# Performance work log

Measured on AMD Instinct MI355X. Metric: run time of the kernel, lower is better.

Reference implementation:

```python
import jax, jax.numpy as jnp
import numpy as np

EPS = 1e-5

def setup_inputs() -> dict:
    key = jax.random.key(0)
    ks = jax.random.split(key, 16)
    B, C, H, W, HID = 32, 512, 56, 56, 128
    inp = {
        "x": jax.random.normal(ks[0], (B, C, H, W), jnp.float32),
        "mod": jax.random.randint(ks[1], (B,), 0, 2, jnp.int32),
        "w1_rgb": jax.random.normal(ks[2], (HID, C), jnp.float32) * 0.05,
        "rm_rgb": jax.random.normal(ks[3], (HID,), jnp.float32) * 0.1,
        "rv_rgb": jax.random.uniform(ks[4], (HID,), jnp.float32, 0.5, 1.5),
        "g_rgb": jax.random.uniform(ks[5], (HID,), jnp.float32, 0.5, 1.5),
        "b_rgb": jax.random.normal(ks[6], (HID,), jnp.float32) * 0.1,
        "w2_rgb": jax.random.normal(ks[7], (C, HID), jnp.float32) * 0.05,
        "w1_inf": jax.random.normal(ks[8], (HID, C), jnp.float32) * 0.05,
        "rm_inf": jax.random.normal(ks[9], (HID,), jnp.float32) * 0.1,
        "rv_inf": jax.random.uniform(ks[10], (HID,), jnp.float32, 0.5, 1.5),
        "g_inf": jax.random.uniform(ks[11], (HID,), jnp.float32, 0.5, 1.5),
        "b_inf": jax.random.normal(ks[12], (HID,), jnp.float32) * 0.1,
        "w2_inf": jax.random.normal(ks[13], (C, HID), jnp.float32) * 0.05,
    }
    return inp

def _branch(x, w1, rm, rv, g, b, w2):
    # 1x1 conv (no bias) -> BN (inference, running stats) -> ReLU -> 1x1 conv
    h = jnp.einsum('bchw,oc->bohw', x, w1)              # (B,HID,H,W)
    scale = g / jnp.sqrt(rv + EPS)                       # (HID,)
    shift = b - rm * scale
    h = jax.nn.relu(h * scale[None, :, None, None] + shift[None, :, None, None])
    return jnp.einsum('bchw,oc->bohw', h, w2)            # (B,C,H,W)

def reference(x, mod, w1_rgb, rm_rgb, rv_rgb, g_rgb, b_rgb, w2_rgb,
              w1_inf, rm_inf, rv_inf, g_inf, b_inf, w2_inf):
    rgb = _branch(x, w1_rgb, rm_rgb, rv_rgb, g_rgb, b_rgb, w2_rgb)
    inf = _branch(x, w1_inf, rm_inf, rv_inf, g_inf, b_inf, w2_inf)
    is_rgb = (mod == 1)[:, None, None, None]
    out = jnp.where(is_rgb, rgb, inf)  # mod in {0,1}; dropout is identity (eval)
    return out
```

## Files before the change

kernel.cpp:

```cpp
#include <hip/hip_runtime.h>
#include <hip/hip_bf16.h>
#include <stdint.h>

#define B_   32
#define C_   512
#define HW_  3136
#define HID_ 128
#define PT   64
#define XP   72
#define HP   136
#define EPS_ 1e-5f

using frag8 = __attribute__((ext_vector_type(8))) short;
using f32x4 = __attribute__((ext_vector_type(4))) float;

__device__ __forceinline__ short f2bf(float f) {
    union { float f; uint32_t u; } v; v.f = f;
    uint32_t u = v.u;
    u += 0x7fffu + ((u >> 16) & 1u);
    return (short)(u >> 16);
}

__global__ __launch_bounds__(256) void prep_kernel(
    const float* __restrict__ w1_rgb, const float* __restrict__ w2_rgb,
    const float* __restrict__ w1_inf, const float* __restrict__ w2_inf,
    const float* __restrict__ rm_rgb, const float* __restrict__ rv_rgb,
    const float* __restrict__ g_rgb,  const float* __restrict__ b_rgb,
    const float* __restrict__ rm_inf, const float* __restrict__ rv_inf,
    const float* __restrict__ g_inf,  const float* __restrict__ b_inf,
    short* __restrict__ w1p_rgb, short* __restrict__ w1p_inf,
    short* __restrict__ w2p_rgb, short* __restrict__ w2p_inf,
    float* __restrict__ ss)
{
    int t = blockIdx.x * 256 + threadIdx.x;
    int p = t >> 9, w = t & 511;
    int q = w >> 7, r = (w >> 3) & 15, j = w & 7;
    {
        int mt = p >> 4, kt = p & 15;
        int m = mt * 16 + r, k = kt * 32 + q * 8 + j;
        w1p_rgb[t] = f2bf(w1_rgb[m * C_ + k]);
        w1p_inf[t] = f2bf(w1_inf[m * C_ + k]);
    }
    {
        int mt = p >> 2, kt = p & 3;
        int m = mt * 16 + r, k = kt * 32 + q * 8 + j;
        w2p_rgb[t] = f2bf(w2_rgb[m * HID_ + k]);
        w2p_inf[t] = f2bf(w2_inf[m * HID_ + k]);
    }
    if (t < 128) {
        float sc = g_rgb[t] * rsqrtf(rv_rgb[t] + EPS_);
        ss[t] = sc; ss[128 + t] = b_rgb[t] - rm_rgb[t] * sc;
    } else if (t < 256) {
        int i = t - 128;
        float sc = g_inf[i] * rsqrtf(rv_inf[i] + EPS_);
        ss[256 + i] = sc; ss[384 + i] = b_inf[i] - rm_inf[i] * sc;
    }
}

__global__ __launch_bounds__(256) void fused_kernel(
    const float* __restrict__ x, const int* __restrict__ mod,
    const short* __restrict__ w1p_rgb, const short* __restrict__ w1p_inf,
    const short* __restrict__ w2p_rgb, const short* __restrict__ w2p_inf,
    const float* __restrict__ ss, float* __restrict__ out)
{
    __shared__ short xlds[PT * XP];
    __shared__ short hlds[PT * HP];

    const int tid  = threadIdx.x;
    const int lane = tid & 63;
    const int wave = tid >> 6;
    const int i16  = lane & 15;
    const int q    = lane >> 4;
    const int b    = blockIdx.y;
    const int p0   = blockIdx.x * PT;

    const int is_rgb = (mod[b] == 1);
    const short* __restrict__ w1p = is_rgb ? w1p_rgb : w1p_inf;
    const short* __restrict__ w2p = is_rgb ? w2p_rgb : w2p_inf;
    const float* __restrict__ scale = ss + (is_rgb ? 0 : 256);
    const float* __restrict__ shift = scale + 128;

    f32x4 acc1[2][4];
    #pragma unroll
    for (int mt = 0; mt < 2; ++mt)
        #pragma unroll
        for (int nt = 0; nt < 4; ++nt)
            acc1[mt][nt] = (f32x4){0.f, 0.f, 0.f, 0.f};

    const int px = tid & 63;
    const int cg = tid >> 6;
    const float* xbase = x + ((size_t)b * C_) * HW_ + p0 + px;

    for (int kc = 0; kc < C_; kc += 64) {
        frag8 af[2][2];
        #pragma unroll
        for (int kk = 0; kk < 2; ++kk) {
            int kt = (kc >> 5) + kk;
            #pragma unroll
            for (int mt = 0; mt < 2; ++mt) {
                int mtg = wave * 2 + mt;
                af[kk][mt] = *(const frag8*)(w1p + ((mtg * 16 + kt) << 9) + lane * 8);
            }
        }
        #pragma unroll
        for (int it = 0; it < 4; ++it) {
            int c = cg * 16 + it * 4;
            float v0 = xbase[(size_t)(kc + c + 0) * HW_];
            float v1 = xbase[(size_t)(kc + c + 1) * HW_];
            float v2 = xbase[(size_t)(kc + c + 2) * HW_];
            float v3 = xbase[(size_t)(kc + c + 3) * HW_];
            short4 pk = make_short4(f2bf(v0), f2bf(v1), f2bf(v2), f2bf(v3));
            *(short4*)(&xlds[px * XP + c]) = pk;
        }
        __syncthreads();
        #pragma unroll
        for (int kk = 0; kk < 2; ++kk) {
            frag8 bfr[4];
            #pragma unroll
            for (int nt = 0; nt < 4; ++nt)
                bfr[nt] = *(const frag8*)(&xlds[(nt * 16 + i16) * XP + kk * 32 + q * 8]);
            #pragma unroll
            for (int mt = 0; mt < 2; ++mt)
                #pragma unroll
                for (int nt = 0; nt < 4; ++nt)
                    acc1[mt][nt] = __builtin_amdgcn_mfma_f32_16x16x32_bf16(
                        af[kk][mt], bfr[nt], acc1[mt][nt], 0, 0, 0);
        }
        __syncthreads();
    }

    #pragma unroll
    for (int mt = 0; mt < 2; ++mt) {
        int mbase = wave * 32 + mt * 16 + q * 4;
        float s0 = scale[mbase + 0], s1 = scale[mbase + 1];
        float s2 = scale[mbase + 2], s3 = scale[mbase + 3];
        float h0 = shift[mbase + 0], h1 = shift[mbase + 1];
        float h2 = shift[mbase + 2], h3 = shift[mbase + 3];
        #pragma unroll
        for (int nt = 0; nt < 4; ++nt) {
            int p = nt * 16 + i16;
            float v0 = fmaxf(acc1[mt][nt][0] * s0 + h0, 0.f);
            float v1 = fmaxf(acc1[mt][nt][1] * s1 + h1, 0.f);
            float v2 = fmaxf(acc1[mt][nt][2] * s2 + h2, 0.f);
            float v3 = fmaxf(acc1[mt][nt][3] * s3 + h3, 0.f);
            short4 pk = make_short4(f2bf(v0), f2bf(v1), f2bf(v2), f2bf(v3));
            *(short4*)(&hlds[p * HP + mbase]) = pk;
        }
    }
    __syncthreads();

    #pragma unroll 1
    for (int half = 0; half < 2; ++half) {
        f32x4 acc2[4][4];
        #pragma unroll
        for (int mt = 0; mt < 4; ++mt)
            #pragma unroll
            for (int nt = 0; nt < 4; ++nt)
                acc2[mt][nt] = (f32x4){0.f, 0.f, 0.f, 0.f};

        #pragma unroll
        for (int kt = 0; kt < 4; ++kt) {
            frag8 af[4], bfr[4];
            #pragma unroll
            for (int mt = 0; mt < 4; ++mt) {
                int mtg = half * 16 + wave * 4 + mt;
                af[mt] = *(const frag8*)(w2p + ((mtg * 4 + kt) << 9) + lane * 8);
            }
            #pragma unroll
            for (int nt = 0; nt < 4; ++nt)
                bfr[nt] = *(const frag8*)(&hlds[(nt * 16 + i16) * HP + kt * 32 + q * 8]);
            #pragma unroll
            for (int mt = 0; mt < 4; ++mt)
                #pragma unroll
                for (int nt = 0; nt < 4; ++nt)
                    acc2[mt][nt] = __builtin_amdgcn_mfma_f32_16x16x32_bf16(
                        af[mt], bfr[nt], acc2[mt][nt], 0, 0, 0);
        }
        #pragma unroll
        for (int mt = 0; mt < 4; ++mt) {
            int mrow = (half * 16 + wave * 4 + mt) * 16 + q * 4;
            #pragma unroll
            for (int nt = 0; nt < 4; ++nt) {
                int col = p0 + nt * 16 + i16;
                float* op = out + ((size_t)(b * C_ + mrow)) * HW_ + col;
                op[0 * HW_] = acc2[mt][nt][0];
                op[1 * HW_] = acc2[mt][nt][1];
                op[2 * HW_] = acc2[mt][nt][2];
                op[3 * HW_] = acc2[mt][nt][3];
            }
        }
    }
}

extern "C" void kernel_launch(void* const* d_in, const int* in_sizes, int n_in,
                              void* d_out, int out_size, void* d_ws, size_t ws_size,
                              hipStream_t stream) {
    const float* x      = (const float*)d_in[0];
    const int*   mod    = (const int*)d_in[1];
    const float* w1_rgb = (const float*)d_in[2];
    const float* rm_rgb = (const float*)d_in[3];
    const float* rv_rgb = (const float*)d_in[4];
    const float* g_rgb  = (const float*)d_in[5];
    const float* b_rgb  = (const float*)d_in[6];
    const float* w2_rgb = (const float*)d_in[7];
    const float* w1_inf = (const float*)d_in[8];
    const float* rm_inf = (const float*)d_in[9];
    const float* rv_inf = (const float*)d_in[10];
    const float* g_inf  = (const float*)d_in[11];
    const float* b_inf  = (const float*)d_in[12];
    const float* w2_inf = (const float*)d_in[13];
    float* out = (float*)d_out;

    char* ws = (char*)d_ws;
    short* w1p_rgb = (short*)(ws + 0);
    short* w1p_inf = (short*)(ws + 131072);
    short* w2p_rgb = (short*)(ws + 262144);
    short* w2p_inf = (short*)(ws + 393216);
    float* ss      = (float*)(ws + 524288);

    prep_kernel<<<256, 256, 0, stream>>>(
        w1_rgb, w2_rgb, w1_inf, w2_inf,
        rm_rgb, rv_rgb, g_rgb, b_rgb,
        rm_inf, rv_inf, g_inf, b_inf,
        w1p_rgb, w1p_inf, w2p_rgb, w2p_inf, ss);

    dim3 grid(HW_ / PT, B_);
    fused_kernel<<<grid, 256, 0, stream>>>(
        x, mod, w1p_rgb, w1p_inf, w2p_rgb, w2p_inf, ss, out);
}
```

Baseline: 385.8 us.

## Double-buffer x staging with register prefetch and vectorize output stores

The first GEMM's x loading now uses two LDS buffers and register prefetch, so global loads for the next 64-channel chunk are issued before the MFMAs on the current chunk, and the per-iteration barrier count drops. Each thread now loads 8 consecutive channels and writes them to LDS as one 16-byte store instead of short4 pieces. The second GEMM swaps the MFMA operand order so each lane holds 4 consecutive pixels, which allows 16-byte nontemporal float4 output stores in place of scalar strided stores. This costs more registers for the prefetch buffers and more LDS.

```diff
diff --git a/kernel.cpp b/kernel.cpp
--- a/kernel.cpp
+++ b/kernel.cpp
@@ -11,8 +11,9 @@
 #define HP   136
 #define EPS_ 1e-5f
 
-using frag8 = __attribute__((ext_vector_type(8))) short;
-using f32x4 = __attribute__((ext_vector_type(4))) float;
+using frag8  = __attribute__((ext_vector_type(8))) short;
+using short8 = __attribute__((ext_vector_type(8))) short;
+using f32x4  = __attribute__((ext_vector_type(4))) float;
 
 __device__ __forceinline__ short f2bf(float f) {
     union { float f; uint32_t u; } v; v.f = f;
@@ -63,7 +64,7 @@
     const short* __restrict__ w2p_rgb, const short* __restrict__ w2p_inf,
     const float* __restrict__ ss, float* __restrict__ out)
 {
-    __shared__ short xlds[PT * XP];
+    __shared__ short xlds[2][PT * XP];
     __shared__ short hlds[PT * HP];
 
     const int tid  = threadIdx.x;
@@ -87,46 +88,100 @@
         for (int nt = 0; nt < 4; ++nt)
             acc1[mt][nt] = (f32x4){0.f, 0.f, 0.f, 0.f};
 
-    const int px = tid & 63;
-    const int cg = tid >> 6;
-    const float* xbase = x + ((size_t)b * C_) * HW_ + p0 + px;
-
-    for (int kc = 0; kc < C_; kc += 64) {
-        frag8 af[2][2];
-        #pragma unroll
-        for (int kk = 0; kk < 2; ++kk) {
-            int kt = (kc >> 5) + kk;
-            #pragma unroll
-            for (int mt = 0; mt < 2; ++mt) {
-                int mtg = wave * 2 + mt;
-                af[kk][mt] = *(const frag8*)(w1p + ((mtg * 16 + kt) << 9) + lane * 8);
-            }
-        }
-        #pragma unroll
-        for (int it = 0; it < 4; ++it) {
-            int c = cg * 16 + it * 4;
-            float v0 = xbase[(size_t)(kc + c + 0) * HW_];
-            float v1 = xbase[(size_t)(kc + c + 1) * HW_];
-            float v2 = xbase[(size_t)(kc + c + 2) * HW_];
-            float v3 = xbase[(size_t)(kc + c + 3) * HW_];
-            short4 pk = make_short4(f2bf(v0), f2bf(v1), f2bf(v2), f2bf(v3));
-            *(short4*)(&xlds[px * XP + c]) = pk;
+    const int px    = lane;
+    const int cbase = wave * 8;
+    const float* __restrict__ xb = x + (size_t)b * C_ * HW_ + p0 + px;
+
+    float rA[16], rB[16];
+    #pragma unroll
+    for (int it = 0; it < 2; ++it)
+        #pragma unroll
+        for (int j = 0; j < 8; ++j)
+            rA[it * 8 + j] = xb[(size_t)(cbase + it * 32 + j) * HW_];
+
+    #pragma unroll 1
+    for (int k2 = 0; k2 < 4; ++k2) {
+        const int kcA = k2 * 2, kcB = kcA + 1;
+
+        #pragma unroll
+        for (int it = 0; it < 2; ++it) {
+            short8 pk;
+            #pragma unroll
+            for (int j = 0; j < 8; ++j) pk[j] = f2bf(rA[it * 8 + j]);
+            *(short8*)(&xlds[0][px * XP + cbase + it * 32]) = pk;
         }
         __syncthreads();
-        #pragma unroll
-        for (int kk = 0; kk < 2; ++kk) {
-            frag8 bfr[4];
-            #pragma unroll
-            for (int nt = 0; nt < 4; ++nt)
-                bfr[nt] = *(const frag8*)(&xlds[(nt * 16 + i16) * XP + kk * 32 + q * 8]);
-            #pragma unroll
-            for (int mt = 0; mt < 2; ++mt)
+
+        #pragma unroll
+        for (int it = 0; it < 2; ++it)
+            #pragma unroll
+            for (int j = 0; j < 8; ++j)
+                rB[it * 8 + j] = xb[(size_t)(kcB * 64 + cbase + it * 32 + j) * HW_];
+
+        {
+            frag8 af[2][2];
+            #pragma unroll
+            for (int kk = 0; kk < 2; ++kk) {
+                int kt = kcA * 2 + kk;
+                #pragma unroll
+                for (int mt = 0; mt < 2; ++mt)
+                    af[kk][mt] = *(const frag8*)(w1p + (((wave * 2 + mt) * 16 + kt) << 9) + lane * 8);
+            }
+            #pragma unroll
+            for (int kk = 0; kk < 2; ++kk) {
+                frag8 bfr[4];
                 #pragma unroll
                 for (int nt = 0; nt < 4; ++nt)
-                    acc1[mt][nt] = __builtin_amdgcn_mfma_f32_16x16x32_bf16(
-                        af[kk][mt], bfr[nt], acc1[mt][nt], 0, 0, 0);
+                    bfr[nt] = *(const frag8*)(&xlds[0][(nt * 16 + i16) * XP + kk * 32 + q * 8]);
+                #pragma unroll
+                for (int mt = 0; mt < 2; ++mt)
+                    #pragma unroll
+                    for (int nt = 0; nt < 4; ++nt)
+                        acc1[mt][nt] = __builtin_amdgcn_mfma_f32_16x16x32_bf16(
+                            af[kk][mt], bfr[nt], acc1[mt][nt], 0, 0, 0);
+            }
+        }
+
+        #pragma unroll
+        for (int it = 0; it < 2; ++it) {
+            short8 pk;
+            #pragma unroll
+            for (int j = 0; j < 8; ++j) pk[j] = f2bf(rB[it * 8 + j]);
+            *(short8*)(&xlds[1][px * XP + cbase + it * 32]) = pk;
         }
         __syncthreads();
+
+        if (k2 < 3) {
+            #pragma unroll
+            for (int it = 0; it < 2; ++it)
+                #pragma unroll
+                for (int j = 0; j < 8; ++j)
+                    rA[it * 8 + j] = xb[(size_t)((kcA + 2) * 64 + cbase + it * 32 + j) * HW_];
+        }
+
+        {
+            frag8 af[2][2];
+            #pragma unroll
+            for (int kk = 0; kk < 2; ++kk) {
+                int kt = kcB * 2 + kk;
+                #pragma unroll
+                for (int mt = 0; mt < 2; ++mt)
+                    af[kk][mt] = *(const frag8*)(w1p + (((wave * 2 + mt) * 16 + kt) << 9) + lane * 8);
+            }
+            #pragma unroll
+            for (int kk = 0; kk < 2; ++kk) {
+                frag8 bfr[4];
+                #pragma unroll
+                for (int nt = 0; nt < 4; ++nt)
+                    bfr[nt] = *(const frag8*)(&xlds[1][(nt * 16 + i16) * XP + kk * 32 + q * 8]);
+                #pragma unroll
+                for (int mt = 0; mt < 2; ++mt)
+                    #pragma unroll
+                    for (int nt = 0; nt < 4; ++nt)
+                        acc1[mt][nt] = __builtin_amdgcn_mfma_f32_16x16x32_bf16(
+                            af[kk][mt], bfr[nt], acc1[mt][nt], 0, 0, 0);
+            }
+        }
     }
 
     #pragma unroll
@@ -139,11 +194,11 @@
         #pragma unroll
         for (int nt = 0; nt < 4; ++nt) {
             int p = nt * 16 + i16;
-            float v0 = fmaxf(acc1[mt][nt][0] * s0 + h0, 0.f);
-            float v1 = fmaxf(acc1[mt][nt][1] * s1 + h1, 0.f);
-            float v2 = fmaxf(acc1[mt][nt][2] * s2 + h2, 0.f);
-            float v3 = fmaxf(acc1[mt][nt][3] * s3 + h3, 0.f);
-            short4 pk = make_short4(f2bf(v0), f2bf(v1), f2bf(v2), f2bf(v3));
+            short4 pk = make_short4(
+                f2bf(fmaxf(acc1[mt][nt][0] * s0 + h0, 0.f)),
+                f2bf(fmaxf(acc1[mt][nt][1] * s1 + h1, 0.f)),
+                f2bf(fmaxf(acc1[mt][nt][2] * s2 + h2, 0.f)),
+                f2bf(fmaxf(acc1[mt][nt][3] * s3 + h3, 0.f)));
             *(short4*)(&hlds[p * HP + mbase]) = pk;
         }
     }
@@ -153,41 +208,37 @@
     for (int half = 0; half < 2; ++half) {
         f32x4 acc2[4][4];
         #pragma unroll
-        for (int mt = 0; mt < 4; ++mt)
-            #pragma unroll
-            for (int nt = 0; nt < 4; ++nt)
-                acc2[mt][nt] = (f32x4){0.f, 0.f, 0.f, 0.f};
+        for (int pt = 0; pt < 4; ++pt)
+            #pragma unroll
+            for (int ct = 0; ct < 4; ++ct)
+                acc2[pt][ct] = (f32x4){0.f, 0.f, 0.f, 0.f};
 
         #pragma unroll
         for (int kt = 0; kt < 4; ++kt) {
-            frag8 af[4], bfr[4];
-            #pragma unroll
-            for (int mt = 0; mt < 4; ++mt) {
-                int mtg = half * 16 + wave * 4 + mt;
-                af[mt] = *(const frag8*)(w2p + ((mtg * 4 + kt) << 9) + lane * 8);
-            }
-            #pragma unroll
-            for (int nt = 0; nt < 4; ++nt)
-                bfr[nt] = *(const frag8*)(&hlds[(nt * 16 + i16) * HP + kt * 32 + q * 8]);
-            #pragma unroll
-            for (int mt = 0; mt < 4; ++mt)
-                #pragma unroll
-                for (int nt = 0; nt < 4; ++nt)
-                    acc2[mt][nt] = __builtin_amdgcn_mfma_f32_16x16x32_bf16(
-                        af[mt], bfr[nt], acc2[mt][nt], 0, 0, 0);
-        }
-        #pragma unroll
-        for (int mt = 0; mt < 4; ++mt) {
-            int mrow = (half * 16 + wave * 4 + mt) * 16 + q * 4;
-            #pragma unroll
-            for (int nt = 0; nt < 4; ++nt) {
-                int col = p0 + nt * 16 + i16;
-                float* op = out + ((size_t)(b * C_ + mrow)) * HW_ + col;
-                op[0 * HW_] = acc2[mt][nt][0];
-                op[1 * HW_] = acc2[mt][nt][1];
-                op[2 * HW_] = acc2[mt][nt][2];
-                op[3 * HW_] = acc2[mt][nt][3];
-            }
+            frag8 wf[4];
+            #pragma unroll
+            for (int ct = 0; ct < 4; ++ct) {
+                int ctg = half * 16 + wave * 4 + ct;
+                wf[ct] = *(const frag8*)(w2p + ((ctg * 4 + kt) << 9) + lane * 8);
+            }
+            frag8 hf[4];
+            #pragma unroll
+            for (int pt = 0; pt < 4; ++pt)
+                hf[pt] = *(const frag8*)(&hlds[(pt * 16 + i16) * HP + kt * 32 + q * 8]);
+            #pragma unroll
+            for (int pt = 0; pt < 4; ++pt)
+                #pragma unroll
+                for (int ct = 0; ct < 4; ++ct)
+                    acc2[pt][ct] = __builtin_amdgcn_mfma_f32_16x16x32_bf16(
+                        hf[pt], wf[ct], acc2[pt][ct], 0, 0, 0);
+        }
+        #pragma unroll
+        for (int ct = 0; ct < 4; ++ct) {
+            int crow = (half * 16 + wave * 4 + ct) * 16 + i16;
+            float* obase = out + ((size_t)(b * C_ + crow)) * HW_ + p0 + q * 4;
+            #pragma unroll
+            for (int pt = 0; pt < 4; ++pt)
+                __builtin_nontemporal_store(acc2[pt][ct], (f32x4*)(obase + pt * 16));
         }
     }
 }
```

Result: slower. 419.4 us (+8.7%).
